# Performance work log

Measured on AMD Instinct MI355X. Metric: run time of the kernel, lower is better.

The kernel has to match this reference:

```python
import jax, jax.numpy as jnp
import numpy as np

WAVEFORM_TICKS = 512
BIN_SIGMA = 5.0
NX, NY = 48, 48
GAUSS_NORM = 0.3989422804  # 1/sqrt(2*pi)
EL_NORM = 2.5066           # sqrt(2*pi) as hard-coded in the module
B, NE = 4, 5000
H1, H2 = 64, 128


def setup_inputs() -> dict:
    key = jax.random.key(0)
    ks = jax.random.split(key, 8)
    simulator_input = 0.5 * jax.random.normal(ks[0], (B, NE, 2), dtype=jnp.float32)
    z_positions = jax.random.uniform(ks[1], (B, NE), dtype=jnp.float32) * (WAVEFORM_TICKS - 1)
    mask = jax.random.uniform(ks[2], (B, NE), dtype=jnp.float32)
    # MLP params: 2 -> 64 -> 128 -> 1
    W1 = jax.random.normal(ks[3], (2, H1), dtype=jnp.float32) * (1.0 / np.sqrt(2.0))
    b1 = jnp.zeros((H1,), jnp.float32)
    W2 = jax.random.normal(ks[4], (H1, H2), dtype=jnp.float32) * (1.0 / np.sqrt(H1))
    b2 = jnp.zeros((H2,), jnp.float32)
    W3 = jax.random.normal(ks[5], (H2, 1), dtype=jnp.float32) * (1.0 / np.sqrt(H2))
    b3 = jnp.zeros((1,), jnp.float32)
    # learned EL spread scalar, init 0.1 as in the module
    el_spread = 0.1 * jnp.ones((1,), jnp.float32)
    # SiPM grid locations in [-1, 1]^2 -> (NX, NY, 2)
    ax = jnp.linspace(-1.0, 1.0, NX, dtype=jnp.float32)
    ay = jnp.linspace(-1.0, 1.0, NY, dtype=jnp.float32)
    gx, gy = jnp.meshgrid(ax, ay, indexing='ij')
    sensor_locations = jnp.stack([gx, gy], axis=-1)
    return {"simulator_input": simulator_input, "z_positions": z_positions, "mask": mask,
            "W1": W1, "b1": b1, "W2": W2, "b2": b2, "W3": W3, "b3": b3,
            "el_spread": el_spread, "sensor_locations": sensor_locations}


def reference(simulator_input, z_positions, mask, W1, b1, W2, b2, W3, b3, el_spread, sensor_locations):
    # MLP per-electron light yield: (B, NE, 2) -> (B, NE)
    h = jax.nn.relu(simulator_input @ W1 + b1)
    h = jax.nn.relu(h @ W2 + b2)
    response = (h @ W3 + b3)[..., 0]

    # spatial gaussian spread onto the sensor grid: (B, NE, NX, NY)
    diff = simulator_input[:, :, None, None, :] - sensor_locations  # (B,NE,NX,NY,2)
    r_squared = jnp.sum(diff * diff, axis=-1)
    es = el_spread[0]
    sipm_spread = 100.0 * jnp.exp(-0.5 * r_squared / (es * es)) / (es * EL_NORM)
    sensor_response = sipm_spread * response[:, :, None, None]  # (B,NE,NX,NY)

    # time-domain gaussian binning: (B, NE, T)
    t = jnp.arange(WAVEFORM_TICKS, dtype=simulator_input.dtype)
    ev = jnp.exp(-((t[None, None, :] - z_positions[..., None]) ** 2) / (2.0 * BIN_SIGMA))
    ev = ev * (GAUSS_NORM / np.sqrt(BIN_SIGMA))
    ev = ev * mask[..., None]

    # contract over electrons: (B,T,NE) x (B,NE,NX*NY) -> (B,T,NX*NY)
    sens_flat = sensor_response.reshape(B, NE, NX * NY)
    wf = jnp.einsum('bet,bes->bts', ev, sens_flat)
    wf = wf.reshape(B, WAVEFORM_TICKS, NX, NY).transpose(0, 2, 3, 1)  # (B,NX,NY,T)
    return wf.sum(axis=0)  # (NX, NY, T)
```

## Files before the change

kernel.cpp:

```cpp
#include <hip/hip_runtime.h>
#include <math.h>

#define NXg 48
#define NYg 48
#define Tg 512
#define NG 20000
#define H1g 64
#define H2g 128

#define TT 32
#define NBINS 16
#define RCAP 3072
#define CCAP (RCAP / 32)
#define SPLIT 3
#define KSPLIT 8
#define NSB 36
#define E2 2
#define EB 256

typedef float vf16 __attribute__((ext_vector_type(16)));
typedef _Float16 half8 __attribute__((ext_vector_type(8)));
typedef float floatx4 __attribute__((ext_vector_type(4)));

#define OFF_BFRAG  0
#define OFF_POSC   (OFF_BFRAG  + (size_t)NBINS*CCAP*4*512*2)
#define OFF_PART   (OFF_POSC   + (size_t)NBINS*RCAP*8)
#define OFF_RESP8  (OFF_PART   + (size_t)SPLIT*NSB*NBINS*2048*4)
#define OFF_EDATA  (OFF_RESP8  + (size_t)NG*8*4)
#define OFF_EDATA2 (OFF_EDATA  + (size_t)NG*16)
#define OFF_LIST   (OFF_EDATA2 + (size_t)NG*16)
#define OFF_CNT    (OFF_LIST   + (size_t)NBINS*RCAP*4)

__global__ __launch_bounds__(EB) void k_mlp(
    const float* __restrict__ sim, const float* __restrict__ zpos,
    const float* __restrict__ mask,
    const float* __restrict__ W1, const float* __restrict__ b1,
    const float* __restrict__ W2, const float* __restrict__ b2,
    const float* __restrict__ W3, const float* __restrict__ b3,
    float4* __restrict__ edata, float* __restrict__ resp8)
{
    __shared__ __align__(64) float sW2[H1g][16];
    __shared__ float4 sW1b[H1g];

    int tid = threadIdx.x;
    int q = blockIdx.y;
    int k0 = q * 16;

    if (tid < H1g)
        sW1b[tid] = make_float4(W1[tid], W1[H1g + tid], b1[tid], 0.0f);
    if (tid < 256) {
        int j = tid >> 2, c = (tid & 3) * 4;
        *(float4*)&sW2[j][c] = *(const float4*)&W2[j * H2g + k0 + c];
    }
    __syncthreads();

    int g0 = blockIdx.x * EB + tid;
    if (g0 >= NG / E2) return;
    int g1 = g0 + NG / E2;

    float2 s0 = *(const float2*)&sim[2 * g0];
    float2 s1 = *(const float2*)&sim[2 * g1];

    vf16 a0 = *(const vf16*)&b2[k0];
    vf16 a1 = a0;
#pragma unroll 4
    for (int j = 0; j < H1g; ++j) {
        float4 wb = sW1b[j];
        float h0 = fmaxf(fmaf(s0.x, wb.x, fmaf(s0.y, wb.y, wb.z)), 0.0f);
        float h1 = fmaxf(fmaf(s1.x, wb.x, fmaf(s1.y, wb.y, wb.z)), 0.0f);
        vf16 w = *(const vf16*)sW2[j];
#pragma unroll
        for (int u = 0; u < 16; ++u) {
            a0[u] = fmaf(h0, w[u], a0[u]);
            a1[u] = fmaf(h1, w[u], a1[u]);
        }
    }

    float r0 = (q == 0) ? b3[0] : 0.0f;
    float r1 = r0;
#pragma unroll
    for (int u = 0; u < 16; ++u) {
        float w3 = W3[k0 + u];
        r0 = fmaf(fmaxf(a0[u], 0.0f), w3, r0);
        r1 = fmaf(fmaxf(a1[u], 0.0f), w3, r1);
    }
    resp8[(size_t)q * NG + g0] = r0;
    resp8[(size_t)q * NG + g1] = r1;

    if (q == 0) {
        edata[g0] = make_float4(s0.x, s0.y, zpos[g0], mask[g0]);
        edata[g1] = make_float4(s1.x, s1.y, zpos[g1], mask[g1]);
    }
}

__global__ __launch_bounds__(256) void k_bins(
    const float* __restrict__ zpos, int* __restrict__ cnt, int* __restrict__ list)
{
    __shared__ int lcnt[NBINS], lbase[NBINS];
    int tid = threadIdx.x;
    if (tid < NBINS) lcnt[tid] = 0;
    __syncthreads();

    int g = blockIdx.x * 256 + tid;
    int jlo = 0, jhi = -1;
    int off[3];
    if (g < NG) {
        float z = zpos[g];
        jlo = max((int)ceilf((z - 44.5f) * (1.0f / 32.0f)), 0);
        jhi = min((int)floorf((z + 13.5f) * (1.0f / 32.0f)), NBINS - 1);
        for (int j = jlo; j <= jhi; ++j)
            off[j - jlo] = atomicAdd(&lcnt[j], 1);
    }
    __syncthreads();
    if (tid < NBINS) {
        int c = lcnt[tid];
        lbase[tid] = c ? atomicAdd(&cnt[tid], c) : 0;
    }
    __syncthreads();
    for (int j = jlo; j <= jhi; ++j) {
        int p = lbase[j] + off[j - jlo];
        if (p < RCAP) list[j * RCAP + p] = g;
    }
}

__global__ __launch_bounds__(256) void k_amp(
    const float4* __restrict__ edata, const float* __restrict__ resp8,
    const float* __restrict__ el_spread, float4* __restrict__ edata2)
{
    int g = blockIdx.x * 256 + threadIdx.x;
    if (g >= NG) return;
    float s = 0.0f;
#pragma unroll
    for (int q = 0; q < KSPLIT; ++q) s += resp8[(size_t)q * NG + g];
    float4 E = edata[g];
    float es = el_spread[0];
    float amp = s * E.w * (100.0f / (es * 2.5066f)) *
                (0.3989422804f / 2.23606797749979f);
    edata2[g] = make_float4(E.x, E.y, E.z, amp);
}

__global__ __launch_bounds__(256) void k_prof(
    const float4* __restrict__ edata2, const int* __restrict__ cnt,
    const int* __restrict__ list,
    _Float16* __restrict__ bfrag, float2* __restrict__ posc)
{
    __shared__ float4 sE[64];
    int bin = blockIdx.y;
    int tid = threadIdx.x;
    int count = min(cnt[bin], RCAP);
    int nch = (count + 31) >> 5;
    int cbase = blockIdx.x * 2;
    if (cbase >= nch) return;

    if (tid < 64) {
        int i = cbase * 32 + tid;
        float4 E = make_float4(1.0e3f, 1.0e3f, 0.0f, 0.0f);
        if (i < count) E = edata2[list[bin * RCAP + i]];
        sE[tid] = E;
        if (i < nch * 32)
            posc[(size_t)bin * RCAP + i] = make_float2(E.x, E.y);
    }
    __syncthreads();

    int ch = cbase + (tid >> 7);
    if (ch >= nch) return;
    int nt = (tid >> 6) & 1;
    int lane = tid & 63;
    int quad = lane >> 4, t16 = lane & 15;
    float tt = (float)(bin * TT + nt * 16 + t16);

    half8 hi, lo;
#pragma unroll
    for (int j = 0; j < 8; ++j) {
        float4 E = sE[(tid >> 7) * 32 + quad * 8 + j];
        float d = tt - E.z;
        float v = E.w * __expf(-0.1f * d * d);
        _Float16 h = (_Float16)v;
        hi[j] = h;
        lo[j] = (_Float16)(v - (float)h);
    }
    size_t base = ((size_t)(bin * CCAP + ch)) * 4 * 512;
    *(half8*)&bfrag[base + (size_t)nt * 512 + lane * 8] = hi;
    *(half8*)&bfrag[base + (size_t)(2 + nt) * 512 + lane * 8] = lo;
}

__global__ __launch_bounds__(256) void k_main(
    const _Float16* __restrict__ bfrag, const float2* __restrict__ posc,
    const int* __restrict__ cnt, const float* __restrict__ el_spread,
    const float* __restrict__ sensors, float* __restrict__ part)
{
    int tid = threadIdx.x;
    int wv = tid >> 6, lane = tid & 63;
    int sb = blockIdx.x, bin = blockIdx.y, split = blockIdx.z;
    int quad = lane >> 4;

    int sA = sb * 64 + wv * 16 + (lane & 15);
    float sxA = sensors[2 * sA], syA = sensors[2 * sA + 1];
    float es = el_spread[0];
    float CL = -0.5f / (es * es);

    int count = min(cnt[bin], RCAP);
    int nch = (count + 31) >> 5;
    int c0 = nch * split / SPLIT, c1 = nch * (split + 1) / SPLIT;

    floatx4 d0 = {0.f, 0.f, 0.f, 0.f}, d1 = {0.f, 0.f, 0.f, 0.f};

    for (int c = c0; c < c1; ++c) {
        const half8* bb = (const half8*)bfrag +
                          ((size_t)(bin * CCAP + c)) * 4 * 64 + lane;
        half8 bh0 = bb[0];
        half8 bh1 = bb[64];
        half8 bl0 = bb[128];
        half8 bl1 = bb[192];

        const float4* pp = (const float4*)(posc +
                           ((size_t)bin * RCAP + c * 32 + quad * 8));
        float4 p0 = pp[0], p1 = pp[1], p2 = pp[2], p3 = pp[3];
        float exs[8] = {p0.x, p0.z, p1.x, p1.z, p2.x, p2.z, p3.x, p3.z};
        float eys[8] = {p0.y, p0.w, p1.y, p1.w, p2.y, p2.w, p3.y, p3.w};

        half8 ah, al;
#pragma unroll
        for (int j = 0; j < 8; ++j) {
            float dx = sxA - exs[j], dy = syA - eys[j];
            float d2 = fmaf(dx, dx, dy * dy);
            float e = __expf(d2 * CL);
            _Float16 h = (_Float16)e;
            ah[j] = h;
            al[j] = (_Float16)(e - (float)h);
        }
        d0 = __builtin_amdgcn_mfma_f32_16x16x32_f16(ah, bh0, d0, 0, 0, 0);
        d1 = __builtin_amdgcn_mfma_f32_16x16x32_f16(ah, bh1, d1, 0, 0, 0);
        d0 = __builtin_amdgcn_mfma_f32_16x16x32_f16(al, bh0, d0, 0, 0, 0);
        d1 = __builtin_amdgcn_mfma_f32_16x16x32_f16(al, bh1, d1, 0, 0, 0);
        d0 = __builtin_amdgcn_mfma_f32_16x16x32_f16(ah, bl0, d0, 0, 0, 0);
        d1 = __builtin_amdgcn_mfma_f32_16x16x32_f16(ah, bl1, d1, 0, 0, 0);
    }

    float* pb = part + (((size_t)split * NSB + sb) * NBINS + bin) * 2048;
    int n0 = lane & 15;
#pragma unroll
    for (int r = 0; r < 4; ++r) {
        int sl = wv * 16 + quad * 4 + r;
        pb[sl * 32 + n0]      = d0[r];
        pb[sl * 32 + 16 + n0] = d1[r];
    }
}

__global__ __launch_bounds__(256) void k_reduce(
    const float4* __restrict__ part, float* __restrict__ out)
{
    int sb = blockIdx.x, bin = blockIdx.y, tid = threadIdx.x;
#pragma unroll
    for (int h = 0; h < 2; ++h) {
        int p = h * 256 + tid;
        int sl = p >> 3, q = p & 7;
        float4 s = make_float4(0.f, 0.f, 0.f, 0.f);
        for (int sp = 0; sp < SPLIT; ++sp) {
            float4 v = part[(((size_t)sp * NSB + sb) * NBINS + bin) * 512 + p];
            s.x += v.x; s.y += v.y; s.z += v.z; s.w += v.w;
        }
        int sensor = sb * 64 + sl;
        *(float4*)(out + (size_t)sensor * Tg + bin * TT + q * 4) = s;
    }
}

extern "C" void kernel_launch(void* const* d_in, const int* in_sizes, int n_in,
                              void* d_out, int out_size, void* d_ws, size_t ws_size,
                              hipStream_t stream)
{
    const float* sim       = (const float*)d_in[0];
    const float* zpos      = (const float*)d_in[1];
    const float* mask      = (const float*)d_in[2];
    const float* W1        = (const float*)d_in[3];
    const float* b1        = (const float*)d_in[4];
    const float* W2        = (const float*)d_in[5];
    const float* b2        = (const float*)d_in[6];
    const float* W3        = (const float*)d_in[7];
    const float* b3        = (const float*)d_in[8];
    const float* el_spread = (const float*)d_in[9];
    const float* sensors   = (const float*)d_in[10];
    float* out = (float*)d_out;

    char* ws = (char*)d_ws;
    _Float16* bfrag  = (_Float16*)(ws + OFF_BFRAG);
    float2*   posc   = (float2*)(ws + OFF_POSC);
    float*    part   = (float*)(ws + OFF_PART);
    float*    resp8  = (float*)(ws + OFF_RESP8);
    float4*   edata  = (float4*)(ws + OFF_EDATA);
    float4*   edata2 = (float4*)(ws + OFF_EDATA2);
    int*      list   = (int*)(ws + OFF_LIST);
    int*      cnt    = (int*)(ws + OFF_CNT);

    hipMemsetAsync(cnt, 0, NBINS * sizeof(int), stream);

    k_mlp<<<dim3((NG / E2 + EB - 1) / EB, KSPLIT), EB, 0, stream>>>(
        sim, zpos, mask, W1, b1, W2, b2, W3, b3, edata, resp8);

    k_bins<<<(NG + 255) / 256, 256, 0, stream>>>(zpos, cnt, list);

    k_amp<<<(NG + 255) / 256, 256, 0, stream>>>(edata, resp8, el_spread, edata2);

    k_prof<<<dim3(CCAP / 2, NBINS), 256, 0, stream>>>(
        edata2, cnt, list, bfrag, posc);

    k_main<<<dim3(NSB, NBINS, SPLIT), 256, 0, stream>>>(
        bfrag, posc, cnt, el_spread, sensors, part);

    k_reduce<<<dim3(NSB, NBINS), 256, 0, stream>>>((const float4*)part, out);
}
```

Before: 145.6 us.

## Fuse amp into binning, drop memset, prescale positions, double-buffer main loop

Merges k_amp into k_bins and zeroes the bin counters inside k_mlp, which removes one kernel launch and the memset. Electron and sensor positions are prescaled by sqrt(0.5*log2 e)/es, so the Gaussian becomes a raw exp2 of the negative squared distance. The k_main chunk loop is software-pipelined with two register buffers so the next chunk's loads overlap the current chunk's MFMAs. Risks include the cnt reset inside k_mlp having to finish before k_bins runs (the kernels are stream-ordered), slightly different exp rounding, and higher register pressure.

```diff
diff --git a/kernel.cpp b/kernel.cpp
--- a/kernel.cpp
+++ b/kernel.cpp
@@ -18,6 +18,8 @@
 #define E2 2
 #define EB 256
 
+#define KSCALE 0.84932180028802f
+
 typedef float vf16 __attribute__((ext_vector_type(16)));
 typedef _Float16 half8 __attribute__((ext_vector_type(8)));
 typedef float floatx4 __attribute__((ext_vector_type(4)));
@@ -37,7 +39,8 @@
     const float* __restrict__ W1, const float* __restrict__ b1,
     const float* __restrict__ W2, const float* __restrict__ b2,
     const float* __restrict__ W3, const float* __restrict__ b3,
-    float4* __restrict__ edata, float* __restrict__ resp8)
+    float4* __restrict__ edata, float* __restrict__ resp8,
+    int* __restrict__ cnt)
 {
     __shared__ __align__(64) float sW2[H1g][16];
     __shared__ float4 sW1b[H1g];
@@ -45,6 +48,8 @@
     int tid = threadIdx.x;
     int q = blockIdx.y;
     int k0 = q * 16;
+
+    if (blockIdx.x == 0 && q == 0 && tid < NBINS) cnt[tid] = 0;
 
     if (tid < H1g)
         sW1b[tid] = make_float4(W1[tid], W1[H1g + tid], b1[tid], 0.0f);
@@ -94,7 +99,9 @@
 }
 
 __global__ __launch_bounds__(256) void k_bins(
-    const float* __restrict__ zpos, int* __restrict__ cnt, int* __restrict__ list)
+    const float4* __restrict__ edata, const float* __restrict__ resp8,
+    const float* __restrict__ el_spread,
+    int* __restrict__ cnt, int* __restrict__ list, float4* __restrict__ edata2)
 {
     __shared__ int lcnt[NBINS], lbase[NBINS];
     int tid = threadIdx.x;
@@ -105,7 +112,17 @@
     int jlo = 0, jhi = -1;
     int off[3];
     if (g < NG) {
-        float z = zpos[g];
+        float4 E = edata[g];
+        float s = 0.0f;
+#pragma unroll
+        for (int q = 0; q < KSPLIT; ++q) s += resp8[(size_t)q * NG + g];
+        float es = el_spread[0];
+        float amp = s * E.w * (100.0f / (es * 2.5066f)) *
+                    (0.3989422804f / 2.23606797749979f);
+        float kk = KSCALE / es;
+        edata2[g] = make_float4(E.x * kk, E.y * kk, E.z, amp);
+
+        float z = E.z;
         jlo = max((int)ceilf((z - 44.5f) * (1.0f / 32.0f)), 0);
         jhi = min((int)floorf((z + 13.5f) * (1.0f / 32.0f)), NBINS - 1);
         for (int j = jlo; j <= jhi; ++j)
@@ -121,22 +138,6 @@
         int p = lbase[j] + off[j - jlo];
         if (p < RCAP) list[j * RCAP + p] = g;
     }
-}
-
-__global__ __launch_bounds__(256) void k_amp(
-    const float4* __restrict__ edata, const float* __restrict__ resp8,
-    const float* __restrict__ el_spread, float4* __restrict__ edata2)
-{
-    int g = blockIdx.x * 256 + threadIdx.x;
-    if (g >= NG) return;
-    float s = 0.0f;
-#pragma unroll
-    for (int q = 0; q < KSPLIT; ++q) s += resp8[(size_t)q * NG + g];
-    float4 E = edata[g];
-    float es = el_spread[0];
-    float amp = s * E.w * (100.0f / (es * 2.5066f)) *
-                (0.3989422804f / 2.23606797749979f);
-    edata2[g] = make_float4(E.x, E.y, E.z, amp);
 }
 
 __global__ __launch_bounds__(256) void k_prof(
@@ -195,9 +196,9 @@
     int quad = lane >> 4;
 
     int sA = sb * 64 + wv * 16 + (lane & 15);
-    float sxA = sensors[2 * sA], syA = sensors[2 * sA + 1];
     float es = el_spread[0];
-    float CL = -0.5f / (es * es);
+    float kk = KSCALE / es;
+    float sxA = sensors[2 * sA] * kk, syA = sensors[2 * sA + 1] * kk;
 
     int count = min(cnt[bin], RCAP);
     int nch = (count + 31) >> 5;
@@ -205,37 +206,55 @@
 
     floatx4 d0 = {0.f, 0.f, 0.f, 0.f}, d1 = {0.f, 0.f, 0.f, 0.f};
 
-    for (int c = c0; c < c1; ++c) {
-        const half8* bb = (const half8*)bfrag +
-                          ((size_t)(bin * CCAP + c)) * 4 * 64 + lane;
-        half8 bh0 = bb[0];
-        half8 bh1 = bb[64];
-        half8 bl0 = bb[128];
-        half8 bl1 = bb[192];
-
-        const float4* pp = (const float4*)(posc +
-                           ((size_t)bin * RCAP + c * 32 + quad * 8));
-        float4 p0 = pp[0], p1 = pp[1], p2 = pp[2], p3 = pp[3];
-        float exs[8] = {p0.x, p0.z, p1.x, p1.z, p2.x, p2.z, p3.x, p3.z};
-        float eys[8] = {p0.y, p0.w, p1.y, p1.w, p2.y, p2.w, p3.y, p3.w};
-
-        half8 ah, al;
-#pragma unroll
-        for (int j = 0; j < 8; ++j) {
-            float dx = sxA - exs[j], dy = syA - eys[j];
-            float d2 = fmaf(dx, dx, dy * dy);
-            float e = __expf(d2 * CL);
-            _Float16 h = (_Float16)e;
-            ah[j] = h;
-            al[j] = (_Float16)(e - (float)h);
+    const half8* bbase = (const half8*)bfrag + (size_t)bin * CCAP * 256 + lane;
+    const float4* pbase = (const float4*)(posc + (size_t)bin * RCAP) + quad * 4;
+
+#define LOADC(c, F0, F1, F2, F3, Q0, Q1, Q2, Q3)                          \
+    {                                                                     \
+        const half8* bb = bbase + (size_t)(c) * 256;                      \
+        F0 = bb[0]; F1 = bb[64]; F2 = bb[128]; F3 = bb[192];              \
+        const float4* pp = pbase + (size_t)(c) * 16;                      \
+        Q0 = pp[0]; Q1 = pp[1]; Q2 = pp[2]; Q3 = pp[3];                   \
+    }
+
+#define COMP(F0, F1, F2, F3, Q0, Q1, Q2, Q3)                              \
+    {                                                                     \
+        float exs[8] = {Q0.x, Q0.z, Q1.x, Q1.z, Q2.x, Q2.z, Q3.x, Q3.z};  \
+        float eys[8] = {Q0.y, Q0.w, Q1.y, Q1.w, Q2.y, Q2.w, Q3.y, Q3.w};  \
+        half8 ah, al;                                                     \
+        _Pragma("unroll")                                                 \
+        for (int j = 0; j < 8; ++j) {                                     \
+            float dx = sxA - exs[j], dy = syA - eys[j];                   \
+            float d2 = fmaf(dy, dy, dx * dx);                             \
+            float e = __builtin_amdgcn_exp2f(-d2);                        \
+            _Float16 h = (_Float16)e;                                     \
+            ah[j] = h;                                                    \
+            al[j] = (_Float16)(e - (float)h);                             \
+        }                                                                 \
+        d0 = __builtin_amdgcn_mfma_f32_16x16x32_f16(ah, F0, d0, 0, 0, 0); \
+        d1 = __builtin_amdgcn_mfma_f32_16x16x32_f16(ah, F1, d1, 0, 0, 0); \
+        d0 = __builtin_amdgcn_mfma_f32_16x16x32_f16(al, F0, d0, 0, 0, 0); \
+        d1 = __builtin_amdgcn_mfma_f32_16x16x32_f16(al, F1, d1, 0, 0, 0); \
+        d0 = __builtin_amdgcn_mfma_f32_16x16x32_f16(ah, F2, d0, 0, 0, 0); \
+        d1 = __builtin_amdgcn_mfma_f32_16x16x32_f16(ah, F3, d1, 0, 0, 0); \
+    }
+
+    if (c0 < c1) {
+        half8 fA0, fA1, fA2, fA3, fB0, fB1, fB2, fB3;
+        float4 qA0, qA1, qA2, qA3, qB0, qB1, qB2, qB3;
+        LOADC(c0, fA0, fA1, fA2, fA3, qA0, qA1, qA2, qA3);
+        int c = c0;
+        for (; c + 1 < c1; c += 2) {
+            LOADC(c + 1, fB0, fB1, fB2, fB3, qB0, qB1, qB2, qB3);
+            COMP(fA0, fA1, fA2, fA3, qA0, qA1, qA2, qA3);
+            int cn = (c + 2 < c1) ? c + 2 : c1 - 1;
+            LOADC(cn, fA0, fA1, fA2, fA3, qA0, qA1, qA2, qA3);
+            COMP(fB0, fB1, fB2, fB3, qB0, qB1, qB2, qB3);
         }
-        d0 = __builtin_amdgcn_mfma_f32_16x16x32_f16(ah, bh0, d0, 0, 0, 0);
-        d1 = __builtin_amdgcn_mfma_f32_16x16x32_f16(ah, bh1, d1, 0, 0, 0);
-        d0 = __builtin_amdgcn_mfma_f32_16x16x32_f16(al, bh0, d0, 0, 0, 0);
-        d1 = __builtin_amdgcn_mfma_f32_16x16x32_f16(al, bh1, d1, 0, 0, 0);
-        d0 = __builtin_amdgcn_mfma_f32_16x16x32_f16(ah, bl0, d0, 0, 0, 0);
-        d1 = __builtin_amdgcn_mfma_f32_16x16x32_f16(ah, bl1, d1, 0, 0, 0);
-    }
+        if (c < c1) COMP(fA0, fA1, fA2, fA3, qA0, qA1, qA2, qA3);
+    }
+#undef LOADC
+#undef COMP
 
     float* pb = part + (((size_t)split * NSB + sb) * NBINS + bin) * 2048;
     int n0 = lane & 15;
@@ -292,14 +311,11 @@
     int*      list   = (int*)(ws + OFF_LIST);
     int*      cnt    = (int*)(ws + OFF_CNT);
 
-    hipMemsetAsync(cnt, 0, NBINS * sizeof(int), stream);
-
     k_mlp<<<dim3((NG / E2 + EB - 1) / EB, KSPLIT), EB, 0, stream>>>(
-        sim, zpos, mask, W1, b1, W2, b2, W3, b3, edata, resp8);
-
-    k_bins<<<(NG + 255) / 256, 256, 0, stream>>>(zpos, cnt, list);
-
-    k_amp<<<(NG + 255) / 256, 256, 0, stream>>>(edata, resp8, el_spread, edata2);
+        sim, zpos, mask, W1, b1, W2, b2, W3, b3, edata, resp8, cnt);
+
+    k_bins<<<(NG + 255) / 256, 256, 0, stream>>>(
+        edata, resp8, el_spread, cnt, list, edata2);
 
     k_prof<<<dim3(CCAP / 2, NBINS), 256, 0, stream>>>(
         edata2, cnt, list, bfrag, posc);
```

Measured after the change: 140.9 us. 1.03x faster.
